# Performance work log

Hardware: AMD Instinct MI355X
Metric: run time of the kernel (lower is better)

The kernel has to match this reference:

```python
import jax, jax.numpy as jnp
import numpy as np

H = 64          # per-direction LSTM hidden
D_IN = 768      # BERT hidden size
D_MODEL = 128   # bidirectional output size


def _lstm_dir(x, W_ih, W_hh, b, reverse):
    # x: [B,S,Din], W_ih: [4H,Din], W_hh: [4H,H], b: [4H]
    B = x.shape[0]
    pre = jnp.einsum('bsd,gd->bsg', x, W_ih) + b  # [B,S,4H]

    def step(carry, p):
        h, c = carry
        g = p + h @ W_hh.T
        i, f, gg, o = jnp.split(g, 4, axis=-1)  # torch gate order i,f,g,o
        c = jax.nn.sigmoid(f) * c + jax.nn.sigmoid(i) * jnp.tanh(gg)
        h = jax.nn.sigmoid(o) * jnp.tanh(c)
        return (h, c), h

    init = (jnp.zeros((B, H), x.dtype), jnp.zeros((B, H), x.dtype))
    _, hs = jax.lax.scan(step, init, jnp.swapaxes(pre, 0, 1), reverse=reverse)
    return jnp.swapaxes(hs, 0, 1)  # [B,S,H]


def _bilstm(x, W_ih, W_hh, b):
    # W_ih: [2,4H,Din] (dir 0 fwd, dir 1 bwd)
    fwd = _lstm_dir(x, W_ih[0], W_hh[0], b[0], False)
    bwd = _lstm_dir(x, W_ih[1], W_hh[1], b[1], True)
    return jnp.concatenate([fwd, bwd], axis=-1)  # [B,S,2H]


def _pool_subwords(subword_emb, word_ids, num_words):
    # scatter-sum subword embeddings into word slots: [B,S,768] -> [B,S,768]
    return jax.vmap(lambda e, i: jax.ops.segment_sum(e, i, num_segments=num_words))(
        subword_emb, word_ids)


def setup_inputs() -> dict:
    key = jax.random.key(0)
    ks = jax.random.split(key, 10)
    B, S = 64, 512
    subword_emb = jax.random.normal(ks[0], (B, S, D_IN), dtype=jnp.float32)
    word_ids_sn = jnp.sort(jax.random.randint(ks[1], (B, S), 0, S, dtype=jnp.int32), axis=1)
    sn_word_len = jax.random.uniform(ks[2], (B, S), dtype=jnp.float32)
    sc = 0.1
    # layer 1: input 768; layers 2-8 (stacked, 7 layers): input 128; combined bias b_ih+b_hh
    W_ih1 = sc * jax.random.normal(ks[3], (2, 4 * H, D_IN), dtype=jnp.float32)
    W_hh1 = sc * jax.random.normal(ks[4], (2, 4 * H, H), dtype=jnp.float32)
    b1 = sc * jax.random.normal(ks[5], (2, 4 * H), dtype=jnp.float32)
    W_ih = sc * jax.random.normal(ks[6], (7, 2, 4 * H, D_MODEL), dtype=jnp.float32)
    W_hh = sc * jax.random.normal(ks[7], (7, 2, 4 * H, H), dtype=jnp.float32)
    b = sc * jax.random.normal(ks[8], (7, 2, 4 * H), dtype=jnp.float32)
    return {"subword_emb": subword_emb, "sn_word_len": sn_word_len,
            "W_ih1": W_ih1, "W_hh1": W_hh1, "b1": b1,
            "W_ih": W_ih, "W_hh": W_hh, "b": b,
            "word_ids_sn": word_ids_sn}


def reference(subword_emb, sn_word_len, W_ih1, W_hh1, b1, W_ih, W_hh, b, word_ids_sn):
    S = subword_emb.shape[1]
    # subword -> word scatter-sum pooling (replaces the per-word-index mask loop)
    merged = _pool_subwords(subword_emb, word_ids_sn, S)        # [B,S,768]
    mask_word = jnp.sum(merged, axis=2).astype(bool)            # [B,S]
    # dropout layers are identity in eval mode
    x = _bilstm(merged, W_ih1, W_hh1, b1)                       # lstm1: 768 -> 128
    x = _bilstm(x, W_ih[0], W_hh[0], b[0])                      # lstm2, no residual
    for l in range(1, 7):                                       # lstm3..lstm8, residual
        x = _bilstm(x, W_ih[l], W_hh[l], b[l]) + x
    out = jnp.concatenate([x, sn_word_len[:, :, None]], axis=2)  # [B,S,129]
    return out, mask_word
```

## Files before the change

kernel.cpp:

```cpp
#include <hip/hip_runtime.h>
#include <math.h>
#include <stdint.h>

#define B 64
#define S 512
#define DIN 768
#define H 64
#define G4 256
#define NG 512
#define DM 128

typedef _Float16 h2_t __attribute__((ext_vector_type(2)));

#if defined(__has_builtin)
#if __has_builtin(__builtin_amdgcn_fdot2)
#define HAS_FDOT2 1
#endif
#endif

__device__ __forceinline__ h2_t u2h(uint32_t u) {
    h2_t h;
    __builtin_memcpy(&h, &u, 4);
    return h;
}

__device__ __forceinline__ float dot2f(h2_t a, h2_t b, float acc) {
#ifdef HAS_FDOT2
    return __builtin_amdgcn_fdot2(a, b, acc, false);
#else
    acc = fmaf((float)a.x, (float)b.x, acc);
    return fmaf((float)a.y, (float)b.y, acc);
#endif
}

__device__ __forceinline__ float sigm(float x) {
    return 1.0f / (1.0f + __expf(-x));
}
__device__ __forceinline__ float tanh_fast(float x) {
    return 1.0f - 2.0f / (__expf(2.0f * x) + 1.0f);
}

__global__ void pool_kernel(const float* __restrict__ emb,
                            const int* __restrict__ ids,
                            float* __restrict__ merged) {
    int b = blockIdx.x;
    int d = blockIdx.y * 128 + threadIdx.x;
    __shared__ int ids_s[S];
    for (int i = threadIdx.x; i < S; i += blockDim.x) ids_s[i] = ids[b * S + i];
    __syncthreads();
    const float* eb = emb + (size_t)b * S * DIN + d;
    float* mb = merged + (size_t)b * S * DIN + d;
    float acc = 0.f;
    for (int s = 0; s < S; ++s) {
        acc += eb[(size_t)s * DIN];
        int id = ids_s[s];
        bool flush = (s == S - 1) || (ids_s[s + 1] != id);
        if (flush) {
            mb[(size_t)id * DIN] = acc;
            acc = 0.f;
        }
    }
}

__global__ void mask_kernel(const float* __restrict__ merged,
                            float* __restrict__ mask) {
    int row = blockIdx.x * 4 + (threadIdx.x >> 6);
    int lane = threadIdx.x & 63;
    const float* r = merged + (size_t)row * DIN;
    float s = 0.f;
    #pragma unroll
    for (int i = 0; i < DIN / 64; ++i) s += r[lane + i * 64];
    #pragma unroll
    for (int off = 32; off > 0; off >>= 1) s += __shfl_down(s, off);
    if (lane == 0) mask[row] = (s != 0.f) ? 1.0f : 0.0f;
}

#define OUTER4(a, w)                                                       \
    acc[0][0] = fmaf(a.x, w.x, acc[0][0]);                                 \
    acc[0][1] = fmaf(a.x, w.y, acc[0][1]);                                 \
    acc[0][2] = fmaf(a.x, w.z, acc[0][2]);                                 \
    acc[0][3] = fmaf(a.x, w.w, acc[0][3]);                                 \
    acc[1][0] = fmaf(a.y, w.x, acc[1][0]);                                 \
    acc[1][1] = fmaf(a.y, w.y, acc[1][1]);                                 \
    acc[1][2] = fmaf(a.y, w.z, acc[1][2]);                                 \
    acc[1][3] = fmaf(a.y, w.w, acc[1][3]);                                 \
    acc[2][0] = fmaf(a.z, w.x, acc[2][0]);                                 \
    acc[2][1] = fmaf(a.z, w.y, acc[2][1]);                                 \
    acc[2][2] = fmaf(a.z, w.z, acc[2][2]);                                 \
    acc[2][3] = fmaf(a.z, w.w, acc[2][3]);                                 \
    acc[3][0] = fmaf(a.w, w.x, acc[3][0]);                                 \
    acc[3][1] = fmaf(a.w, w.y, acc[3][1]);                                 \
    acc[3][2] = fmaf(a.w, w.z, acc[3][2]);                                 \
    acc[3][3] = fmaf(a.w, w.w, acc[3][3]);

__global__ __launch_bounds__(256, 2) void gemm_nt_bias(
    const float* __restrict__ A, int K,
    const float* __restrict__ Wt, const float* __restrict__ bias,
    float* __restrict__ C) {
    __shared__ __align__(16) float As[16][68];
    __shared__ __align__(16) float Bs[16][68];
    int tid = threadIdx.x;
    int m0 = blockIdx.x * 64;
    int n0 = blockIdx.y * 64;
    int lr = tid >> 2;
    int lk = (tid & 3) << 2;
    int tx = tid & 15, ty = tid >> 4;
    float acc[4][4] = {};
    const float* Ap = A + (size_t)(m0 + lr) * K + lk;
    const float* Wp = Wt + (size_t)(n0 + lr) * K + lk;

    float4 av = *(const float4*)(Ap);
    float4 wv = *(const float4*)(Wp);
    for (int k0 = 0; k0 < K; k0 += 16) {
        As[lk + 0][lr] = av.x; As[lk + 1][lr] = av.y;
        As[lk + 2][lr] = av.z; As[lk + 3][lr] = av.w;
        Bs[lk + 0][lr] = wv.x; Bs[lk + 1][lr] = wv.y;
        Bs[lk + 2][lr] = wv.z; Bs[lk + 3][lr] = wv.w;
        __syncthreads();
        float4 av2 = av, wv2 = wv;
        if (k0 + 16 < K) {
            av2 = *(const float4*)(Ap + k0 + 16);
            wv2 = *(const float4*)(Wp + k0 + 16);
        }
        #pragma unroll
        for (int k = 0; k < 16; ++k) {
            float4 a = *(const float4*)&As[k][ty << 2];
            float4 w = *(const float4*)&Bs[k][tx << 2];
            OUTER4(a, w);
        }
        __syncthreads();
        av = av2; wv = wv2;
    }
    float4 bv = *(const float4*)&bias[n0 + (tx << 2)];
    #pragma unroll
    for (int i = 0; i < 4; ++i) {
        float4 r;
        r.x = acc[i][0] + bv.x;
        r.y = acc[i][1] + bv.y;
        r.z = acc[i][2] + bv.z;
        r.w = acc[i][3] + bv.w;
        *(float4*)&C[(size_t)(m0 + (ty << 2) + i) * NG + n0 + (tx << 2)] = r;
    }
}

__global__ __launch_bounds__(64, 1) void lstm_rec(
    const float* __restrict__ pre,
    const float* __restrict__ Whh,
    const float* __restrict__ xin,
    float* __restrict__ xout,
    int residual) {
    int b = blockIdx.x >> 1;
    int dir = blockIdx.x & 1;
    int j = threadIdx.x & 63;

    h2_t wg0[32], wg1[32], wg2[32], wg3[32];
    {
        const float* w0 = Whh + (size_t)(dir * G4 + 0 * H + j) * H;
        const float* w1 = Whh + (size_t)(dir * G4 + 1 * H + j) * H;
        const float* w2 = Whh + (size_t)(dir * G4 + 2 * H + j) * H;
        const float* w3 = Whh + (size_t)(dir * G4 + 3 * H + j) * H;
        #pragma unroll
        for (int kk = 0; kk < 32; ++kk) {
            float2 v;
            h2_t p;
            v = *(const float2*)&w0[kk * 2];
            p.x = (_Float16)v.x; p.y = (_Float16)v.y; wg0[kk] = p;
            v = *(const float2*)&w1[kk * 2];
            p.x = (_Float16)v.x; p.y = (_Float16)v.y; wg1[kk] = p;
            v = *(const float2*)&w2[kk * 2];
            p.x = (_Float16)v.x; p.y = (_Float16)v.y; wg2[kk] = p;
            v = *(const float2*)&w3[kk * 2];
            p.x = (_Float16)v.x; p.y = (_Float16)v.y; wg3[kk] = p;
        }
    }

    const float* preb = pre + (size_t)b * S * NG + dir * G4 + j;
    const float* xinb = xin + (size_t)b * S * DM + dir * H + j;
    float* xoutb = xout + (size_t)b * S * DM + dir * H + j;

    float pi[4], pf[4], pg_[4], po[4], rb[4] = {0.f, 0.f, 0.f, 0.f};
    #pragma unroll
    for (int i = 0; i < 4; ++i) {
        int s = dir ? (S - 1 - i) : i;
        const float* p = preb + (size_t)s * NG;
        pi[i] = p[0];
        pf[i] = p[64];
        pg_[i] = p[128];
        po[i] = p[192];
        if (residual) rb[i] = xinb[(size_t)s * DM];
    }

    __shared__ __align__(16) _Float16 shh[64];
    shh[j] = (_Float16)0.f;

    float c = 0.f;
    #pragma unroll 4
    for (int step = 0; step < S; ++step) {
        int s = dir ? (S - 1 - step) : step;
        int q = step & 3;
        float ai = pi[q], af = pf[q], ag = pg_[q], ao = po[q];
        float rv = rb[q];
        int sn = step + 4;
        if (sn < S) {
            int s2 = dir ? (S - 1 - sn) : sn;
            const float* p = preb + (size_t)s2 * NG;
            pi[q] = p[0];
            pf[q] = p[64];
            pg_[q] = p[128];
            po[q] = p[192];
            if (residual) rb[q] = xinb[(size_t)s2 * DM];
        }

        uint4 hq[8];
        const uint4* hp = (const uint4*)shh;
        #pragma unroll
        for (int r = 0; r < 8; ++r) hq[r] = hp[r];

        #pragma unroll
        for (int r = 0; r < 8; ++r) {
            uint32_t uu[4] = {hq[r].x, hq[r].y, hq[r].z, hq[r].w};
            #pragma unroll
            for (int cc = 0; cc < 4; ++cc) {
                int kk = r * 4 + cc;
                h2_t hh = u2h(uu[cc]);
                ai = dot2f(hh, wg0[kk], ai);
                af = dot2f(hh, wg1[kk], af);
                ag = dot2f(hh, wg2[kk], ag);
                ao = dot2f(hh, wg3[kk], ao);
            }
        }
        c = sigm(af) * c + sigm(ai) * tanh_fast(ag);
        float h = sigm(ao) * tanh_fast(c);
        shh[j] = (_Float16)h;
        xoutb[(size_t)s * DM] = h + rv;
    }
}

__global__ void assemble_kernel(const float* __restrict__ x,
                                const float* __restrict__ wl,
                                float* __restrict__ out0) {
    int idx = blockIdx.x * blockDim.x + threadIdx.x;
    if (idx >= B * S * 129) return;
    int c = idx % 129;
    int bs = idx / 129;
    out0[idx] = (c < 128) ? x[(size_t)bs * DM + c] : wl[bs];
}

extern "C" void kernel_launch(void* const* d_in, const int* in_sizes, int n_in,
                              void* d_out, int out_size, void* d_ws, size_t ws_size,
                              hipStream_t stream) {
    const float* emb  = (const float*)d_in[0];
    const float* wl   = (const float*)d_in[1];
    const float* Wih1 = (const float*)d_in[2];
    const float* Whh1 = (const float*)d_in[3];
    const float* b1   = (const float*)d_in[4];
    const float* Wih  = (const float*)d_in[5];
    const float* Whh  = (const float*)d_in[6];
    const float* bb   = (const float*)d_in[7];
    const int*   ids  = (const int*)d_in[8];

    float* out0 = (float*)d_out;
    float* mask_out = out0 + (size_t)B * S * 129;

    float* merged = (float*)d_ws;
    float* pre    = merged + (size_t)B * S * DIN;
    float* xA     = pre + (size_t)B * S * NG;
    float* xB     = xA + (size_t)B * S * DM;

    hipMemsetAsync(merged, 0, (size_t)B * S * DIN * sizeof(float), stream);
    pool_kernel<<<dim3(B, 6), 128, 0, stream>>>(emb, ids, merged);
    mask_kernel<<<(B * S) / 4, 256, 0, stream>>>(merged, mask_out);

    dim3 ggrid(512, 8);

    gemm_nt_bias<<<ggrid, 256, 0, stream>>>(merged, DIN, Wih1, b1, pre);
    lstm_rec<<<2 * B, 64, 0, stream>>>(pre, Whh1, nullptr, xA, 0);

    gemm_nt_bias<<<ggrid, 256, 0, stream>>>(xA, DM, Wih, bb, pre);
    lstm_rec<<<2 * B, 64, 0, stream>>>(pre, Whh, nullptr, xB, 0);

    float* cur = xB;
    float* oth = xA;
    for (int l = 1; l < 7; ++l) {
        gemm_nt_bias<<<ggrid, 256, 0, stream>>>(cur, DM, Wih + (size_t)l * NG * DM,
                                                bb + (size_t)l * NG, pre);
        lstm_rec<<<2 * B, 64, 0, stream>>>(pre, Whh + (size_t)l * NG * H,
                                           cur, oth, 1);
        float* tmp = cur; cur = oth; oth = tmp;
    }

    assemble_kernel<<<(B * S * 129 + 255) / 256, 256, 0, stream>>>(cur, wl, out0);
}
```

Measured before the change: 3.066 ms.

## Replace FP32 SIMT input-projection GEMM with FP16 MFMA tiled kernel

The input-projection GEMM now converts A and W tiles to half precision in shared memory and uses 16x16x32 f16 MFMA instructions. Each block computes a 128x64 output tile with four waves. The aim is to remove the FP32 FMA-bound cost of the per-layer GEMMs. In exchange, inputs are rounded to fp16, which reduces accuracy, and the global loads are no longer prefetched.

```diff
diff --git a/kernel.cpp b/kernel.cpp
--- a/kernel.cpp
+++ b/kernel.cpp
@@ -11,6 +11,8 @@
 #define DM 128
 
 typedef _Float16 h2_t __attribute__((ext_vector_type(2)));
+typedef _Float16 f16x8 __attribute__((ext_vector_type(8)));
+typedef float f32x4 __attribute__((ext_vector_type(4)));
 
 #if defined(__has_builtin)
 #if __has_builtin(__builtin_amdgcn_fdot2)
@@ -75,71 +77,90 @@
     if (lane == 0) mask[row] = (s != 0.f) ? 1.0f : 0.0f;
 }
 
-#define OUTER4(a, w)                                                       \
-    acc[0][0] = fmaf(a.x, w.x, acc[0][0]);                                 \
-    acc[0][1] = fmaf(a.x, w.y, acc[0][1]);                                 \
-    acc[0][2] = fmaf(a.x, w.z, acc[0][2]);                                 \
-    acc[0][3] = fmaf(a.x, w.w, acc[0][3]);                                 \
-    acc[1][0] = fmaf(a.y, w.x, acc[1][0]);                                 \
-    acc[1][1] = fmaf(a.y, w.y, acc[1][1]);                                 \
-    acc[1][2] = fmaf(a.y, w.z, acc[1][2]);                                 \
-    acc[1][3] = fmaf(a.y, w.w, acc[1][3]);                                 \
-    acc[2][0] = fmaf(a.z, w.x, acc[2][0]);                                 \
-    acc[2][1] = fmaf(a.z, w.y, acc[2][1]);                                 \
-    acc[2][2] = fmaf(a.z, w.z, acc[2][2]);                                 \
-    acc[2][3] = fmaf(a.z, w.w, acc[2][3]);                                 \
-    acc[3][0] = fmaf(a.w, w.x, acc[3][0]);                                 \
-    acc[3][1] = fmaf(a.w, w.y, acc[3][1]);                                 \
-    acc[3][2] = fmaf(a.w, w.z, acc[3][2]);                                 \
-    acc[3][3] = fmaf(a.w, w.w, acc[3][3]);
-
-__global__ __launch_bounds__(256, 2) void gemm_nt_bias(
+#define LDK 40
+
+__global__ __launch_bounds__(256, 2) void gemm_mfma(
     const float* __restrict__ A, int K,
     const float* __restrict__ Wt, const float* __restrict__ bias,
     float* __restrict__ C) {
-    __shared__ __align__(16) float As[16][68];
-    __shared__ __align__(16) float Bs[16][68];
+    __shared__ __align__(16) _Float16 Alds[128][LDK];
+    __shared__ __align__(16) _Float16 Blds[64][LDK];
     int tid = threadIdx.x;
-    int m0 = blockIdx.x * 64;
-    int n0 = blockIdx.y * 64;
-    int lr = tid >> 2;
-    int lk = (tid & 3) << 2;
-    int tx = tid & 15, ty = tid >> 4;
-    float acc[4][4] = {};
-    const float* Ap = A + (size_t)(m0 + lr) * K + lk;
-    const float* Wp = Wt + (size_t)(n0 + lr) * K + lk;
-
-    float4 av = *(const float4*)(Ap);
-    float4 wv = *(const float4*)(Wp);
-    for (int k0 = 0; k0 < K; k0 += 16) {
-        As[lk + 0][lr] = av.x; As[lk + 1][lr] = av.y;
-        As[lk + 2][lr] = av.z; As[lk + 3][lr] = av.w;
-        Bs[lk + 0][lr] = wv.x; Bs[lk + 1][lr] = wv.y;
-        Bs[lk + 2][lr] = wv.z; Bs[lk + 3][lr] = wv.w;
+    int lane = tid & 63;
+    int wave = tid >> 6;
+    int wm = wave >> 1, wn = wave & 1;
+    int n0 = blockIdx.x * 64;
+    int m0 = blockIdx.y * 128;
+
+    int tr = tid >> 2;
+    int tc = (tid & 3) << 3;
+
+    f32x4 acc[4][2] = {};
+
+    const float* Ab = A + (size_t)m0 * K;
+    for (int k0 = 0; k0 < K; k0 += 32) {
+        {
+            const float* src = Ab + (size_t)tr * K + k0 + tc;
+            float4 v0 = *(const float4*)(src);
+            float4 v1 = *(const float4*)(src + 4);
+            _Float16* dst = &Alds[tr][tc];
+            dst[0] = (_Float16)v0.x; dst[1] = (_Float16)v0.y;
+            dst[2] = (_Float16)v0.z; dst[3] = (_Float16)v0.w;
+            dst[4] = (_Float16)v1.x; dst[5] = (_Float16)v1.y;
+            dst[6] = (_Float16)v1.z; dst[7] = (_Float16)v1.w;
+            src += (size_t)64 * K;
+            float4 v2 = *(const float4*)(src);
+            float4 v3 = *(const float4*)(src + 4);
+            dst = &Alds[tr + 64][tc];
+            dst[0] = (_Float16)v2.x; dst[1] = (_Float16)v2.y;
+            dst[2] = (_Float16)v2.z; dst[3] = (_Float16)v2.w;
+            dst[4] = (_Float16)v3.x; dst[5] = (_Float16)v3.y;
+            dst[6] = (_Float16)v3.z; dst[7] = (_Float16)v3.w;
+        }
+        {
+            const float* src = Wt + (size_t)(n0 + tr) * K + k0 + tc;
+            float4 v0 = *(const float4*)(src);
+            float4 v1 = *(const float4*)(src + 4);
+            _Float16* dst = &Blds[tr][tc];
+            dst[0] = (_Float16)v0.x; dst[1] = (_Float16)v0.y;
+            dst[2] = (_Float16)v0.z; dst[3] = (_Float16)v0.w;
+            dst[4] = (_Float16)v1.x; dst[5] = (_Float16)v1.y;
+            dst[6] = (_Float16)v1.z; dst[7] = (_Float16)v1.w;
+        }
         __syncthreads();
-        float4 av2 = av, wv2 = wv;
-        if (k0 + 16 < K) {
-            av2 = *(const float4*)(Ap + k0 + 16);
-            wv2 = *(const float4*)(Wp + k0 + 16);
-        }
-        #pragma unroll
-        for (int k = 0; k < 16; ++k) {
-            float4 a = *(const float4*)&As[k][ty << 2];
-            float4 w = *(const float4*)&Bs[k][tx << 2];
-            OUTER4(a, w);
-        }
+
+        int fr = lane & 15;
+        int kg = (lane >> 4) << 3;
+        f16x8 af[4], bf[2];
+        #pragma unroll
+        for (int mf = 0; mf < 4; ++mf)
+            af[mf] = *(const f16x8*)&Alds[wm * 64 + mf * 16 + fr][kg];
+        #pragma unroll
+        for (int nf = 0; nf < 2; ++nf)
+            bf[nf] = *(const f16x8*)&Blds[wn * 32 + nf * 16 + fr][kg];
+        #pragma unroll
+        for (int mf = 0; mf < 4; ++mf)
+            #pragma unroll
+            for (int nf = 0; nf < 2; ++nf)
+                acc[mf][nf] = __builtin_amdgcn_mfma_f32_16x16x32_f16(
+                    af[mf], bf[nf], acc[mf][nf], 0, 0, 0);
         __syncthreads();
-        av = av2; wv = wv2;
-    }
-    float4 bv = *(const float4*)&bias[n0 + (tx << 2)];
+    }
+
+    int col = lane & 15;
+    int r4 = (lane >> 4) << 2;
     #pragma unroll
-    for (int i = 0; i < 4; ++i) {
-        float4 r;
-        r.x = acc[i][0] + bv.x;
-        r.y = acc[i][1] + bv.y;
-        r.z = acc[i][2] + bv.z;
-        r.w = acc[i][3] + bv.w;
-        *(float4*)&C[(size_t)(m0 + (ty << 2) + i) * NG + n0 + (tx << 2)] = r;
+    for (int nf = 0; nf < 2; ++nf) {
+        int n = n0 + wn * 32 + nf * 16 + col;
+        float bv = bias[n];
+        #pragma unroll
+        for (int mf = 0; mf < 4; ++mf) {
+            #pragma unroll
+            for (int reg = 0; reg < 4; ++reg) {
+                int m = m0 + wm * 64 + mf * 16 + r4 + reg;
+                C[(size_t)m * NG + n] = acc[mf][nf][reg] + bv;
+            }
+        }
     }
 }
 
@@ -271,19 +292,19 @@
     pool_kernel<<<dim3(B, 6), 128, 0, stream>>>(emb, ids, merged);
     mask_kernel<<<(B * S) / 4, 256, 0, stream>>>(merged, mask_out);
 
-    dim3 ggrid(512, 8);
-
-    gemm_nt_bias<<<ggrid, 256, 0, stream>>>(merged, DIN, Wih1, b1, pre);
+    dim3 ggrid(NG / 64, (B * S) / 128);
+
+    gemm_mfma<<<ggrid, 256, 0, stream>>>(merged, DIN, Wih1, b1, pre);
     lstm_rec<<<2 * B, 64, 0, stream>>>(pre, Whh1, nullptr, xA, 0);
 
-    gemm_nt_bias<<<ggrid, 256, 0, stream>>>(xA, DM, Wih, bb, pre);
+    gemm_mfma<<<ggrid, 256, 0, stream>>>(xA, DM, Wih, bb, pre);
     lstm_rec<<<2 * B, 64, 0, stream>>>(pre, Whh, nullptr, xB, 0);
 
     float* cur = xB;
     float* oth = xA;
     for (int l = 1; l < 7; ++l) {
-        gemm_nt_bias<<<ggrid, 256, 0, stream>>>(cur, DM, Wih + (size_t)l * NG * DM,
-                                                bb + (size_t)l * NG, pre);
+        gemm_mfma<<<ggrid, 256, 0, stream>>>(cur, DM, Wih + (size_t)l * NG * DM,
+                                             bb + (size_t)l * NG, pre);
         lstm_rec<<<2 * B, 64, 0, stream>>>(pre, Whh + (size_t)l * NG * H,
                                            cur, oth, 1);
         float* tmp = cur; cur = oth; oth = tmp;
```

Result: faster. 2.685 ms (-12.4%).
